# Performance work log

Hardware: AMD Instinct MI355X
Metric: run time of the kernel (lower is better)

The kernel has to match this reference:

```python
import jax, jax.numpy as jnp
import numpy as np

B, S, D = 2, 4096, 512
H = 8
HD = D // H


def setup_inputs() -> dict:
    key = jax.random.key(0)
    k1, k2, k3, k4, k5 = jax.random.split(key, 5)
    sd = 1.0 / np.sqrt(D)
    return {
        "x": jax.random.normal(k1, (B, S, D), dtype=jnp.float32),
        "Wqkv": jax.random.normal(k2, (3 * D, D), dtype=jnp.float32) * sd,
        "bqkv": jax.random.normal(k3, (3 * D,), dtype=jnp.float32) * 0.02,
        "Wo": jax.random.normal(k4, (D, D), dtype=jnp.float32) * sd,
        "bo": jax.random.normal(k5, (D,), dtype=jnp.float32) * 0.02,
    }


def reference(x, Wqkv, bqkv, Wo, bo):
    b, s, d = x.shape
    h, hd = H, d // H
    # QKV projection (torch Linear: x @ W^T + b)
    qkv = x @ Wqkv.T + bqkv                      # [b, s, 3d]
    q, k, v = jnp.split(qkv, 3, axis=-1)         # each [b, s, d]
    # [b, s, h, hd] -> [b, h, s, hd]
    q = q.reshape(b, s, h, hd).transpose(0, 2, 1, 3)
    k = k.reshape(b, s, h, hd).transpose(0, 2, 1, 3)
    v = v.reshape(b, s, h, hd).transpose(0, 2, 1, 3)
    # causal additive mask: triu(ones, diag=1) * -1e10
    mask = jnp.triu(jnp.ones((s, s), dtype=x.dtype), k=1) * jnp.asarray(-1e10, x.dtype)
    wts = jnp.einsum("bhqd,bhkd->bhqk", q, k) / np.sqrt(hd).astype(np.float32)
    wts = wts + mask[None, None, :, :]
    wts = jax.nn.softmax(wts, axis=-1)
    y = jnp.einsum("bhqk,bhkd->bhqd", wts, v)    # [b, h, s, hd]
    y = y.transpose(0, 2, 1, 3).reshape(b, s, d) # [b, s, d]
    out = y @ Wo.T + bo
    return out
```

## Files before the change

### kernel.cpp

```cpp
#include <hip/hip_runtime.h>


typedef __bf16 bf16x8 __attribute__((ext_vector_type(8)));
typedef float f32x4 __attribute__((ext_vector_type(4)));
typedef unsigned short u16;

#define MFMA(a, b, c) __builtin_amdgcn_mfma_f32_16x16x32_bf16(a, b, c, 0, 0, 0)
#define QSCALE 0.18033688011112042f

__device__ __forceinline__ float exp2_fast(float x) {
    return __builtin_amdgcn_exp2f(x);
}
__device__ __forceinline__ u16 f2bf(float f) {
    union { __bf16 h; u16 u; } v; v.h = (__bf16)f; return v.u;
}
__device__ __forceinline__ ushort4 f4_to_bf4(float4 v) {
    ushort4 r;
    r.x = f2bf(v.x); r.y = f2bf(v.y); r.z = f2bf(v.z); r.w = f2bf(v.w);
    return r;
}
__device__ __forceinline__ void load_lds16(const u16* g, u16* l) {
    __builtin_amdgcn_global_load_lds(
        (const __attribute__((address_space(1))) void*)g,
        (__attribute__((address_space(3))) void*)l, 16, 0, 0);
}

__global__ __launch_bounds__(256) void cvt_all(
    const float* __restrict__ x, const float* __restrict__ wq,
    const float* __restrict__ wo,
    u16* __restrict__ xb, u16* __restrict__ wqb, u16* __restrict__ wob)
{
    int i = blockIdx.x * 256 + threadIdx.x;
    if (i < 1048576) {
        ((ushort4*)xb)[i] = f4_to_bf4(((const float4*)x)[i]);
    } else if (i < 1048576 + 196608) {
        int j = i - 1048576;
        ((ushort4*)wqb)[j] = f4_to_bf4(((const float4*)wq)[j]);
    } else {
        int j = i - 1048576 - 196608;
        ((ushort4*)wob)[j] = f4_to_bf4(((const float4*)wo)[j]);
    }
}

__global__ __launch_bounds__(256) void gemm_qkv_bf(
    const u16* __restrict__ X, const u16* __restrict__ W,
    const float* __restrict__ bias,
    u16* __restrict__ QY, u16* __restrict__ Kf, u16* __restrict__ Vf)
{
    __shared__ u16 As[2 * 128 * 32];
    __shared__ u16 Bs[2 * 128 * 32];
    const int K = 512;
    const int tid = threadIdx.x, wave = tid >> 6, lane = tid & 63;
    const int l15 = lane & 15, quad = lane >> 4;
    const int bm = blockIdx.x * 128, bn = blockIdx.y * 128;
    const bool vmode = (bn >= 1024);
    const int wr = wave >> 1, wc = wave & 1;
    const int arow = lane >> 2;
    const int acol = (lane & 3) * 8;

    f32x4 acc[4][4] = {};
#pragma unroll
    for (int ii = 0; ii < 2; ii++) {
        const int inst = wave * 2 + ii;
        const int row = inst * 16 + arow;
        load_lds16(&X[(bm + row) * K + acol], &As[inst * 512]);
        load_lds16(&W[(bn + row) * K + acol], &Bs[inst * 512]);
    }
    int cur = 0;
    for (int k0 = 0; k0 < K; k0 += 32) {
        __builtin_amdgcn_s_barrier();
        if (k0 + 32 < K) {
            const int nb = (cur ^ 1) * 4096;
#pragma unroll
            for (int ii = 0; ii < 2; ii++) {
                const int inst = wave * 2 + ii;
                const int row = inst * 16 + arow;
                load_lds16(&X[(bm + row) * K + k0 + 32 + acol], &As[nb + inst * 512]);
                load_lds16(&W[(bn + row) * K + k0 + 32 + acol], &Bs[nb + inst * 512]);
            }
            asm volatile("s_waitcnt vmcnt(4)" ::: "memory");
        } else {
            asm volatile("s_waitcnt vmcnt(0)" ::: "memory");
        }
        __builtin_amdgcn_s_barrier();
        const int cb = cur * 4096;
        bf16x8 a[4], b[4];
#pragma unroll
        for (int i = 0; i < 4; i++)
            a[i] = *(const bf16x8*)&As[cb + (wr * 64 + i * 16 + l15) * 32 + quad * 8];
#pragma unroll
        for (int j = 0; j < 4; j++)
            b[j] = *(const bf16x8*)&Bs[cb + (wc * 64 + j * 16 + l15) * 32 + quad * 8];
        if (vmode) {
#pragma unroll
            for (int i = 0; i < 4; i++)
#pragma unroll
                for (int j = 0; j < 4; j++)
                    acc[i][j] = MFMA(a[j], b[i], acc[i][j]);
        } else {
#pragma unroll
            for (int i = 0; i < 4; i++)
#pragma unroll
                for (int j = 0; j < 4; j++)
                    acc[i][j] = MFMA(b[i], a[j], acc[i][j]);
        }
        cur ^= 1;
    }

    const int nbase = bn + wc * 64;
    if (vmode) {
#pragma unroll
        for (int i = 0; i < 4; i++) {
            const int d0 = nbase + i * 16 + l15;
            const float bvf = bias[d0];
            const int d0m = d0 & 511;
            const int h = d0m >> 6, hd0 = d0m & 63;
            const int n = hd0 >> 4, lv = hd0 & 15;
#pragma unroll
            for (int j = 0; j < 4; j++) {
                const int s_g = bm + wr * 64 + j * 16 + quad * 4;
                const int b_ = s_g >> 12, s0 = s_g & 4095;
                const int kt = s0 >> 6, kk = s0 & 63;
                const int half = kk >> 5, qv = (kk >> 3) & 3, e0 = kk & 7;
                ushort4 pk;
                pk.x = f2bf(acc[i][j][0] + bvf);
                pk.y = f2bf(acc[i][j][1] + bvf);
                pk.z = f2bf(acc[i][j][2] + bvf);
                pk.w = f2bf(acc[i][j][3] + bvf);
                const size_t off = ((size_t)((b_ * 8 + h) * 64 + kt)) * 4096 +
                                   n * 1024 + half * 512 + qv * 128 + lv * 8 + e0;
                *(ushort4*)&Vf[off] = pk;
            }
        }
    } else {
        const int which = nbase >> 9;
#pragma unroll
        for (int i = 0; i < 4; i++) {
            const int d0 = nbase + i * 16 + quad * 4;
            const float4 bv = *(const float4*)&bias[d0];
            const int d0m = d0 & 511;
            const int h = d0m >> 6, hd0 = d0m & 63;
#pragma unroll
            for (int j = 0; j < 4; j++) {
                const int s_g = bm + wr * 64 + j * 16 + l15;
                const int b_ = s_g >> 12, s0 = s_g & 4095;
                const int bhh = b_ * 8 + h;
                const int kt = s0 >> 6;
                if (which == 1) {
                    const int jj = (s0 >> 4) & 3, lr = s0 & 15;
                    const int half = hd0 >> 5, q4 = (hd0 >> 3) & 3, e0 = hd0 & 7;
                    ushort4 pk;
                    pk.x = f2bf(acc[i][j][0] + bv.x);
                    pk.y = f2bf(acc[i][j][1] + bv.y);
                    pk.z = f2bf(acc[i][j][2] + bv.z);
                    pk.w = f2bf(acc[i][j][3] + bv.w);
                    const size_t off = ((size_t)(bhh * 64 + kt)) * 4096 +
                                       jj * 1024 + half * 512 + q4 * 128 + lr * 8 + e0;
                    *(ushort4*)&Kf[off] = pk;
                } else {
                    ushort4 pk;
                    pk.x = f2bf((acc[i][j][0] + bv.x) * QSCALE);
                    pk.y = f2bf((acc[i][j][1] + bv.y) * QSCALE);
                    pk.z = f2bf((acc[i][j][2] + bv.z) * QSCALE);
                    pk.w = f2bf((acc[i][j][3] + bv.w) * QSCALE);
                    *(ushort4*)&QY[((b_ * 4096 + s0) * 8 + h) * 64 + hd0] = pk;
                }
            }
        }
    }
}

#define LS 72

#define GLD(dst, base, OFF)                                                  \
    asm volatile("global_load_dwordx4 %0, %1, off offset:" #OFF              \
                 : "=v"(dst) : "v"(base))

#define WAITV(N) do {                                                        \
    asm volatile("s_waitcnt vmcnt(" #N ")" ::: "memory");                    \
    __builtin_amdgcn_sched_barrier(0);                                       \
} while (0)

__global__ __launch_bounds__(64, 2) void attn_k(
    const u16* __restrict__ QY, const u16* __restrict__ Kf, const u16* __restrict__ Vf,
    u16* __restrict__ PO, float* __restrict__ ML)
{
    __shared__ u16 Ps[16 * LS];

    const int lane = threadIdx.x;
    const int l15 = lane & 15, quad = lane >> 4;
    const int bh = blockIdx.x;
    const int b_ = bh >> 3, h = bh & 7;
    const int y = (int)blockIdx.y;
    const int p = y >> 1;
    const int seg = y & 1;

    bf16x8 ones;
#pragma unroll
    for (int i = 0; i < 8; i++) ones[i] = (__bf16)1.0f;

    const u16* KfB = &Kf[((size_t)bh * 64) * 4096 + lane * 8];
    const u16* VfB = &Vf[((size_t)bh * 64) * 4096 + lane * 8];
    u16* P = Ps;

#define LOADK(DK, KT) do {                                                   \
    const u16* ka_ = KfB + (size_t)(KT) * 4096;                              \
    const u16* kb_ = ka_ + 2048;                                             \
    GLD(DK[0][0], ka_, 0);    GLD(DK[0][1], ka_, 1024);                      \
    GLD(DK[1][0], ka_, 2048); GLD(DK[1][1], ka_, 3072);                      \
    GLD(DK[2][0], kb_, 0);    GLD(DK[2][1], kb_, 1024);                      \
    GLD(DK[3][0], kb_, 2048); GLD(DK[3][1], kb_, 3072);                      \
} while (0)

#define LOADV(DV, KT) do {                                                   \
    const u16* va_ = VfB + (size_t)(KT) * 4096;                              \
    const u16* vb_ = va_ + 2048;                                             \
    GLD(DV[0][0], va_, 0);    GLD(DV[0][1], va_, 1024);                      \
    GLD(DV[1][0], va_, 2048); GLD(DV[1][1], va_, 3072);                      \
    GLD(DV[2][0], vb_, 0);    GLD(DV[2][1], vb_, 1024);                      \
    GLD(DV[3][0], vb_, 2048); GLD(DV[3][1], vb_, 3072);                      \
} while (0)

#define TILE_A(KC, KT) do {                                                  \
    const int k0_ = (KT) * 64;                                               \
    const bool nmA_ = (k0_ + 63 > base_r);                                   \
    const bool nmB_ = (k0_ + 63 > base_r + 16);                              \
    f32x4 sa_[4], sb_[4];                                                    \
    _Pragma("unroll")                                                        \
    for (int j_ = 0; j_ < 4; j_++) {                                         \
        f32x4 ia_ = {}, ib_ = {};                                            \
        if (nmA_) {                                                          \
            _Pragma("unroll")                                                \
            for (int r_ = 0; r_ < 4; r_++) {                                 \
                const int key_ = k0_ + j_ * 16 + quad * 4 + r_;              \
                ia_[r_] = (key_ > rowA) ? -1e30f : 0.0f;                     \
            }                                                                \
        }                                                                    \
        if (nmB_) {                                                          \
            _Pragma("unroll")                                                \
            for (int r_ = 0; r_ < 4; r_++) {                                 \
                const int key_ = k0_ + j_ * 16 + quad * 4 + r_;              \
                ib_[r_] = (key_ > rowA + 16) ? -1e30f : 0.0f;                \
            }                                                                \
        }                                                                    \
        ia_ = MFMA(KC[j_][0], qa0, ia_);                                     \
        sa_[j_] = MFMA(KC[j_][1], qa1, ia_);                                 \
        ib_ = MFMA(KC[j_][0], qb0, ib_);                                     \
        sb_[j_] = MFMA(KC[j_][1], qb1, ib_);                                 \
    }                                                                        \
    _Pragma("unroll")                                                        \
    for (int j_ = 0; j_ < 4; j_++) {                                         \
        ushort4 w_;                                                          \
        w_.x = f2bf(exp2_fast(sa_[j_][0]));                                  \
        w_.y = f2bf(exp2_fast(sa_[j_][1]));                                  \
        w_.z = f2bf(exp2_fast(sa_[j_][2]));                                  \
        w_.w = f2bf(exp2_fast(sa_[j_][3]));                                  \
        *(ushort4*)&P[l15 * LS + j_ * 16 + quad * 4] = w_;                   \
    }                                                                        \
    _Pragma("unroll")                                                        \
    for (int j_ = 0; j_ < 4; j_++)                                           \
        _Pragma("unroll")                                                    \
        for (int r_ = 0; r_ < 4; r_++)                                       \
            spb[j_][r_] = exp2_fast(sb_[j_][r_]);                            \
    pfa0 = *(const bf16x8*)&P[l15 * LS + quad * 8];                          \
    pfa1 = *(const bf16x8*)&P[l15 * LS + 32 + quad * 8];                     \
    _Pragma("unroll")                                                        \
    for (int j_ = 0; j_ < 4; j_++) {                                         \
        ushort4 w_;                                                          \
        w_.x = f2bf(spb[j_][0]); w_.y = f2bf(spb[j_][1]);                    \
        w_.z = f2bf(spb[j_][2]); w_.w = f2bf(spb[j_][3]);                    \
        *(ushort4*)&P[l15 * LS + j_ * 16 + quad * 4] = w_;                   \
    }                                                                        \
} while (0)

#define TILE_B(VC) do {                                                      \
    lacc_a = MFMA(ones, pfa0, lacc_a);                                       \
    lacc_a = MFMA(ones, pfa1, lacc_a);                                       \
    _Pragma("unroll")                                                        \
    for (int n_ = 0; n_ < 4; n_++) {                                         \
        oa[n_] = MFMA(VC[n_][0], pfa0, oa[n_]);                              \
        oa[n_] = MFMA(VC[n_][1], pfa1, oa[n_]);                              \
    }                                                                        \
    bf16x8 pfb0_ = *(const bf16x8*)&P[l15 * LS + quad * 8];                  \
    bf16x8 pfb1_ = *(const bf16x8*)&P[l15 * LS + 32 + quad * 8];             \
    lacc_b = MFMA(ones, pfb0_, lacc_b);                                      \
    lacc_b = MFMA(ones, pfb1_, lacc_b);                                      \
    _Pragma("unroll")                                                        \
    for (int n_ = 0; n_ < 4; n_++) {                                         \
        ob[n_] = MFMA(VC[n_][0], pfb0_, ob[n_]);                             \
        ob[n_] = MFMA(VC[n_][1], pfb1_, ob[n_]);                             \
    }                                                                        \
} while (0)

    for (int phase = 0; phase < 2; phase++) {
        const int qt32 = phase ? (127 - p) : p;
        const int nt = (qt32 >> 1) + 1;
        const int hlf = (nt + 1) >> 1;
        const int t0 = seg ? hlf : 0;
        const int t1 = seg ? nt : hlf;
        const int base_r = qt32 * 32;

        const u16* qpa = &QY[((b_ * 4096 + base_r + l15) * 8 + h) * 64 + quad * 8];
        const u16* qpb = qpa + 16 * 8 * 64;
        bf16x8 qa0, qa1, qb0, qb1;
        GLD(qa0, qpa, 0);
        GLD(qa1, qpa, 64);
        GLD(qb0, qpb, 0);
        GLD(qb1, qpb, 64);

        f32x4 oa[4] = {}, ob[4] = {};
        f32x4 lacc_a = {}, lacc_b = {};
        const int rowA = base_r + l15;

        float spb[4][4];
        bf16x8 pfa0, pfa1;
        bf16x8 kR[4][2], kS[4][2], vv[4][2];

        if (t0 < t1) LOADK(kR, t0);
        for (int kt = t0; kt < t1; kt += 2) {
            const bool h1 = (kt + 1 < t1);
            LOADV(vv, kt);
            if (h1) LOADK(kS, kt + 1);
            if (h1) { WAITV(16); } else { WAITV(8); }
            TILE_A(kR, kt);
            if (h1) { WAITV(8); } else { WAITV(0); }
            TILE_B(vv);
            if (h1) {
                const bool h2 = (kt + 2 < t1);
                LOADV(vv, kt + 1);
                if (h2) LOADK(kR, kt + 2);
                if (h2) { WAITV(16); } else { WAITV(8); }
                TILE_A(kS, kt + 1);
                if (h2) { WAITV(8); } else { WAITV(0); }
                TILE_B(vv);
            }
        }

        u16* ppa = &PO[(size_t)seg * 4194304 +
                       (size_t)((b_ * 4096 + base_r + l15) * 8 + h) * 64];
        u16* ppb = ppa + 16 * 8 * 64;
#pragma unroll
        for (int n = 0; n < 4; n++) {
            ushort4 wa;
            wa.x = f2bf(oa[n][0]);
            wa.y = f2bf(oa[n][1]);
            wa.z = f2bf(oa[n][2]);
            wa.w = f2bf(oa[n][3]);
            *(ushort4*)&ppa[n * 16 + quad * 4] = wa;
            ushort4 wb;
            wb.x = f2bf(ob[n][0]);
            wb.y = f2bf(ob[n][1]);
            wb.z = f2bf(ob[n][2]);
            wb.w = f2bf(ob[n][3]);
            *(ushort4*)&ppb[n * 16 + quad * 4] = wb;
        }
        if (quad == 0) {
            ML[(seg * 16 + bh) * 4096 + base_r + l15] = lacc_a[0];
            ML[(seg * 16 + bh) * 4096 + base_r + 16 + l15] = lacc_b[0];
        }
    }
#undef LOADK
#undef LOADV
#undef TILE_A
#undef TILE_B
}

__global__ __launch_bounds__(256) void merge_k(
    const u16* __restrict__ PO, const float* __restrict__ ML, u16* __restrict__ Y)
{
    const int flat = blockIdx.x * 256 + threadIdx.x;
    const int rs = flat >> 6;
    const int rem = flat & 63;
    const int h = rem >> 3, c = rem & 7;
    const int b_ = rs >> 12, s = rs & 4095;
    const int bh = b_ * 8 + h;
    const float l0 = ML[bh * 4096 + s];
    const float l1 = ML[(16 + bh) * 4096 + s];
    const float inv = 1.0f / (l0 + l1);

    const size_t base = (size_t)(rs * 8 + h) * 64 + c * 8;
    bf16x8 x0 = *(const bf16x8*)&PO[base];
    bf16x8 x1 = *(const bf16x8*)&PO[4194304 + base];
    ushort4 lo, hi;
    lo.x = f2bf(((float)x0[0] + (float)x1[0]) * inv);
    lo.y = f2bf(((float)x0[1] + (float)x1[1]) * inv);
    lo.z = f2bf(((float)x0[2] + (float)x1[2]) * inv);
    lo.w = f2bf(((float)x0[3] + (float)x1[3]) * inv);
    hi.x = f2bf(((float)x0[4] + (float)x1[4]) * inv);
    hi.y = f2bf(((float)x0[5] + (float)x1[5]) * inv);
    hi.z = f2bf(((float)x0[6] + (float)x1[6]) * inv);
    hi.w = f2bf(((float)x0[7] + (float)x1[7]) * inv);
    *(ushort4*)&Y[base] = lo;
    *(ushort4*)&Y[base + 4] = hi;
}

__global__ __launch_bounds__(256) void gemm_o_bf(
    const u16* __restrict__ X, const u16* __restrict__ W,
    const float* __restrict__ bias, float* __restrict__ Out)
{
    __shared__ u16 As[2 * 128 * 32];
    __shared__ u16 Bs[2 * 128 * 32];
    const int K = 512;
    const int tid = threadIdx.x, wave = tid >> 6, lane = tid & 63;
    const int l15 = lane & 15, quad = lane >> 4;
    const int bm = blockIdx.x * 128, bn = blockIdx.y * 128;
    const int wr = wave >> 1, wc = wave & 1;
    const int arow = lane >> 2;
    const int acol = (lane & 3) * 8;

    f32x4 acc[4][4] = {};
#pragma unroll
    for (int ii = 0; ii < 2; ii++) {
        const int inst = wave * 2 + ii;
        const int row = inst * 16 + arow;
        load_lds16(&X[(bm + row) * K + acol], &As[inst * 512]);
        load_lds16(&W[(bn + row) * K + acol], &Bs[inst * 512]);
    }
    int cur = 0;
    for (int k0 = 0; k0 < K; k0 += 32) {
        __builtin_amdgcn_s_barrier();
        if (k0 + 32 < K) {
            const int nb = (cur ^ 1) * 4096;
#pragma unroll
            for (int ii = 0; ii < 2; ii++) {
                const int inst = wave * 2 + ii;
                const int row = inst * 16 + arow;
                load_lds16(&X[(bm + row) * K + k0 + 32 + acol], &As[nb + inst * 512]);
                load_lds16(&W[(bn + row) * K + k0 + 32 + acol], &Bs[nb + inst * 512]);
            }
            asm volatile("s_waitcnt vmcnt(4)" ::: "memory");
        } else {
            asm volatile("s_waitcnt vmcnt(0)" ::: "memory");
        }
        __builtin_amdgcn_s_barrier();
        const int cb = cur * 4096;
        bf16x8 a[4], b[4];
#pragma unroll
        for (int i = 0; i < 4; i++)
            a[i] = *(const bf16x8*)&As[cb + (wr * 64 + i * 16 + l15) * 32 + quad * 8];
#pragma unroll
        for (int j = 0; j < 4; j++)
            b[j] = *(const bf16x8*)&Bs[cb + (wc * 64 + j * 16 + l15) * 32 + quad * 8];
#pragma unroll
        for (int i = 0; i < 4; i++)
#pragma unroll
            for (int j = 0; j < 4; j++)
                acc[i][j] = MFMA(b[i], a[j], acc[i][j]);
        cur ^= 1;
    }
#pragma unroll
    for (int i = 0; i < 4; i++) {
        const int n0 = bn + wc * 64 + i * 16 + quad * 4;
        const float4 bv = *(const float4*)&bias[n0];
#pragma unroll
        for (int j = 0; j < 4; j++) {
            const int m = bm + wr * 64 + j * 16 + l15;
            float4 ov;
            ov.x = acc[i][j][0] + bv.x;
            ov.y = acc[i][j][1] + bv.y;
            ov.z = acc[i][j][2] + bv.z;
            ov.w = acc[i][j][3] + bv.w;
            *(float4*)&Out[(size_t)m * 512 + n0] = ov;
        }
    }
}

extern "C" void kernel_launch(void* const* d_in, const int* in_sizes, int n_in,
                              void* d_out, int out_size, void* d_ws, size_t ws_size,
                              hipStream_t stream) {
    (void)in_sizes; (void)n_in; (void)out_size; (void)ws_size;
    const float* x    = (const float*)d_in[0];
    const float* Wqkv = (const float*)d_in[1];
    const float* bqkv = (const float*)d_in[2];
    const float* Wo   = (const float*)d_in[3];
    const float* bo   = (const float*)d_in[4];
    float* out = (float*)d_out;

    u16* qy_ws = (u16*)d_ws;
    u16* kf_ws = qy_ws + 4194304;
    u16* vf_ws = kf_ws + 4194304;
    float* ml  = (float*)(vf_ws + 4194304);
    u16* wqkvb = (u16*)(ml + 262144);
    u16* wob   = wqkvb + 786432;
    u16* xb    = (u16*)d_out;
    u16* po    = (u16*)d_out;

    cvt_all<<<5120, 256, 0, stream>>>(x, Wqkv, Wo, xb, wqkvb, wob);
    gemm_qkv_bf<<<dim3(64, 12), 256, 0, stream>>>(xb, wqkvb, bqkv, qy_ws, kf_ws, vf_ws);
    attn_k<<<dim3(16, 128), 64, 0, stream>>>(qy_ws, kf_ws, vf_ws, po, ml);
    merge_k<<<2048, 256, 0, stream>>>(po, ml, qy_ws);
    gemm_o_bf<<<dim3(64, 4), 256, 0, stream>>>(qy_ws, wob, bo, out);
}
```

Baseline: 179.1 us.

## Fuse split-KV merge into attention kernel via two waves per block

The two KV segments previously handled by separate single-wave blocks are now handled by two waves of one block. Their partial outputs and row sums are combined through LDS and normalized in-kernel, which removes the merge kernel and the round trip of partial outputs and ML through global memory. The attention output is written in place into the QY buffer. The cost is an LDS exchange plus barriers per row tile, and wave 0 alone does the final write. Per-block LDS and thread count also grow, which may change occupancy.

```diff
diff --git a/kernel.cpp b/kernel.cpp
--- a/kernel.cpp
+++ b/kernel.cpp
@@ -181,19 +181,21 @@
     __builtin_amdgcn_sched_barrier(0);                                       \
 } while (0)
 
-__global__ __launch_bounds__(64, 2) void attn_k(
-    const u16* __restrict__ QY, const u16* __restrict__ Kf, const u16* __restrict__ Vf,
-    u16* __restrict__ PO, float* __restrict__ ML)
+__global__ __launch_bounds__(128, 2) void attn_k(
+    u16* __restrict__ QY, const u16* __restrict__ Kf, const u16* __restrict__ Vf)
 {
-    __shared__ u16 Ps[16 * LS];
-
-    const int lane = threadIdx.x;
+    __shared__ u16 Ps[2 * 16 * LS];
+    __shared__ float OxA[4][64][4];
+    __shared__ float OxB[4][64][4];
+    __shared__ float Lx[64][2];
+
+    const int tid = threadIdx.x;
+    const int wave = tid >> 6, lane = tid & 63;
     const int l15 = lane & 15, quad = lane >> 4;
     const int bh = blockIdx.x;
     const int b_ = bh >> 3, h = bh & 7;
-    const int y = (int)blockIdx.y;
-    const int p = y >> 1;
-    const int seg = y & 1;
+    const int p = (int)blockIdx.y;
+    const int seg = wave;
 
     bf16x8 ones;
 #pragma unroll
@@ -201,7 +203,7 @@
 
     const u16* KfB = &Kf[((size_t)bh * 64) * 4096 + lane * 8];
     const u16* VfB = &Vf[((size_t)bh * 64) * 4096 + lane * 8];
-    u16* P = Ps;
+    u16* P = &Ps[wave * 16 * LS];
 
 #define LOADK(DK, KT) do {                                                   \
     const u16* ka_ = KfB + (size_t)(KT) * 4096;                              \
@@ -336,62 +338,47 @@
             }
         }
 
-        u16* ppa = &PO[(size_t)seg * 4194304 +
-                       (size_t)((b_ * 4096 + base_r + l15) * 8 + h) * 64];
-        u16* ppb = ppa + 16 * 8 * 64;
-#pragma unroll
-        for (int n = 0; n < 4; n++) {
-            ushort4 wa;
-            wa.x = f2bf(oa[n][0]);
-            wa.y = f2bf(oa[n][1]);
-            wa.z = f2bf(oa[n][2]);
-            wa.w = f2bf(oa[n][3]);
-            *(ushort4*)&ppa[n * 16 + quad * 4] = wa;
-            ushort4 wb;
-            wb.x = f2bf(ob[n][0]);
-            wb.y = f2bf(ob[n][1]);
-            wb.z = f2bf(ob[n][2]);
-            wb.w = f2bf(ob[n][3]);
-            *(ushort4*)&ppb[n * 16 + quad * 4] = wb;
-        }
-        if (quad == 0) {
-            ML[(seg * 16 + bh) * 4096 + base_r + l15] = lacc_a[0];
-            ML[(seg * 16 + bh) * 4096 + base_r + 16 + l15] = lacc_b[0];
-        }
+        if (wave == 1) {
+#pragma unroll
+            for (int n = 0; n < 4; n++) {
+                *(f32x4*)&OxA[n][lane][0] = oa[n];
+                *(f32x4*)&OxB[n][lane][0] = ob[n];
+            }
+            Lx[lane][0] = lacc_a[0];
+            Lx[lane][1] = lacc_b[0];
+        }
+        __syncthreads();
+        if (wave == 0) {
+            const float la = lacc_a[0] + Lx[lane][0];
+            const float lb = lacc_b[0] + Lx[lane][1];
+            const float iva = (la > 0.0f) ? 1.0f / la : 0.0f;
+            const float ivb = (lb > 0.0f) ? 1.0f / lb : 0.0f;
+            u16* ya = &QY[((size_t)((b_ * 4096 + base_r + l15) * 8 + h)) * 64];
+            u16* yb = ya + 16 * 8 * 64;
+#pragma unroll
+            for (int n = 0; n < 4; n++) {
+                f32x4 sa4 = *(const f32x4*)&OxA[n][lane][0];
+                f32x4 sb4 = *(const f32x4*)&OxB[n][lane][0];
+                ushort4 wa;
+                wa.x = f2bf((oa[n][0] + sa4[0]) * iva);
+                wa.y = f2bf((oa[n][1] + sa4[1]) * iva);
+                wa.z = f2bf((oa[n][2] + sa4[2]) * iva);
+                wa.w = f2bf((oa[n][3] + sa4[3]) * iva);
+                *(ushort4*)&ya[n * 16 + quad * 4] = wa;
+                ushort4 wb;
+                wb.x = f2bf((ob[n][0] + sb4[0]) * ivb);
+                wb.y = f2bf((ob[n][1] + sb4[1]) * ivb);
+                wb.z = f2bf((ob[n][2] + sb4[2]) * ivb);
+                wb.w = f2bf((ob[n][3] + sb4[3]) * ivb);
+                *(ushort4*)&yb[n * 16 + quad * 4] = wb;
+            }
+        }
+        __syncthreads();
     }
 #undef LOADK
 #undef LOADV
 #undef TILE_A
 #undef TILE_B
-}
-
-__global__ __launch_bounds__(256) void merge_k(
-    const u16* __restrict__ PO, const float* __restrict__ ML, u16* __restrict__ Y)
-{
-    const int flat = blockIdx.x * 256 + threadIdx.x;
-    const int rs = flat >> 6;
-    const int rem = flat & 63;
-    const int h = rem >> 3, c = rem & 7;
-    const int b_ = rs >> 12, s = rs & 4095;
-    const int bh = b_ * 8 + h;
-    const float l0 = ML[bh * 4096 + s];
-    const float l1 = ML[(16 + bh) * 4096 + s];
-    const float inv = 1.0f / (l0 + l1);
-
-    const size_t base = (size_t)(rs * 8 + h) * 64 + c * 8;
-    bf16x8 x0 = *(const bf16x8*)&PO[base];
-    bf16x8 x1 = *(const bf16x8*)&PO[4194304 + base];
-    ushort4 lo, hi;
-    lo.x = f2bf(((float)x0[0] + (float)x1[0]) * inv);
-    lo.y = f2bf(((float)x0[1] + (float)x1[1]) * inv);
-    lo.z = f2bf(((float)x0[2] + (float)x1[2]) * inv);
-    lo.w = f2bf(((float)x0[3] + (float)x1[3]) * inv);
-    hi.x = f2bf(((float)x0[4] + (float)x1[4]) * inv);
-    hi.y = f2bf(((float)x0[5] + (float)x1[5]) * inv);
-    hi.z = f2bf(((float)x0[6] + (float)x1[6]) * inv);
-    hi.w = f2bf(((float)x0[7] + (float)x1[7]) * inv);
-    *(ushort4*)&Y[base] = lo;
-    *(ushort4*)&Y[base + 4] = hi;
 }
 
 __global__ __launch_bounds__(256) void gemm_o_bf(
@@ -483,11 +470,9 @@
     u16* wqkvb = (u16*)(ml + 262144);
     u16* wob   = wqkvb + 786432;
     u16* xb    = (u16*)d_out;
-    u16* po    = (u16*)d_out;
 
     cvt_all<<<5120, 256, 0, stream>>>(x, Wqkv, Wo, xb, wqkvb, wob);
     gemm_qkv_bf<<<dim3(64, 12), 256, 0, stream>>>(xb, wqkvb, bqkv, qy_ws, kf_ws, vf_ws);
-    attn_k<<<dim3(16, 128), 64, 0, stream>>>(qy_ws, kf_ws, vf_ws, po, ml);
-    merge_k<<<2048, 256, 0, stream>>>(po, ml, qy_ws);
+    attn_k<<<dim3(16, 64), 128, 0, stream>>>(qy_ws, kf_ws, vf_ws);
     gemm_o_bf<<<dim3(64, 4), 256, 0, stream>>>(qy_ws, wob, bo, out);
 }
```

Result: faster. 174.3 us (median of 2 runs) (-2.7%).
